# Optimization experiments

Measured on AMD Instinct MI355X. Metric: run time of the kernel, lower is better.

## Reference

```python
import jax, jax.numpy as jnp
import numpy as np

B, T, C = 4, 2048, 2048
N_HEAD = 16
HEAD_DIM = C // N_HEAD
ROPE_BASE = 10000.0


def setup_inputs() -> dict:
    key = jax.random.key(0)
    k1, k2, k3 = jax.random.split(key, 3)
    x = jax.random.normal(k1, (B, T, C), dtype=jnp.float32)
    Wqkv = jax.random.normal(k2, (C, 3 * C), dtype=jnp.float32) * 0.02
    bqkv = jnp.zeros((3 * C,), dtype=jnp.float32)
    Wproj = jax.random.normal(k3, (C, C), dtype=jnp.float32) * 0.02
    bproj = jnp.zeros((C,), dtype=jnp.float32)
    return {"x": x, "Wqkv": Wqkv, "bqkv": bqkv, "Wproj": Wproj, "bproj": bproj}


def _rope_cos_sin(seq_len, head_dim, dtype):
    inv_freq = 1.0 / (ROPE_BASE ** (jnp.arange(0, head_dim, 2, dtype=jnp.float32) / head_dim))
    t = jnp.arange(seq_len, dtype=jnp.float32)
    freqs = jnp.einsum("i,j->ij", t, inv_freq)          # [T, D/2]
    emb = jnp.concatenate([freqs, freqs], axis=-1)       # [T, D]
    return jnp.cos(emb).astype(dtype), jnp.sin(emb).astype(dtype)


def _rotate_half(x):
    half = x.shape[-1] // 2
    x1, x2 = x[..., :half], x[..., half:]
    return jnp.concatenate([-x2, x1], axis=-1)


def reference(x, Wqkv, bqkv, Wproj, bproj):
    b, t, c = x.shape
    qkv = x @ Wqkv + bqkv                                # [B, T, 3C]
    q, k, v = jnp.split(qkv, 3, axis=-1)
    # [B, T, C] -> [B, H, T, D]
    def to_heads(u):
        return u.reshape(b, t, N_HEAD, HEAD_DIM).transpose(0, 2, 1, 3)
    q, k, v = to_heads(q), to_heads(k), to_heads(v)
    cos, sin = _rope_cos_sin(t, HEAD_DIM, x.dtype)       # [T, D]
    cos = cos[None, None]                                # [1, 1, T, D]
    sin = sin[None, None]
    q = q * cos + _rotate_half(q) * sin
    k = k * cos + _rotate_half(k) * sin
    scale = 1.0 / np.sqrt(HEAD_DIM).astype(np.float32)
    scores = jnp.einsum("bhqd,bhkd->bhqk", q, k) * scale  # [B, H, T, T]
    causal = jnp.tril(jnp.ones((t, t), dtype=bool))
    scores = jnp.where(causal[None, None], scores, jnp.finfo(scores.dtype).min)
    att = jax.nn.softmax(scores, axis=-1)
    y = jnp.einsum("bhqk,bhkd->bhqd", att, v)             # [B, H, T, D]
    y = y.transpose(0, 2, 1, 3).reshape(b, t, c)
    return y @ Wproj + bproj
```

## Files before the change

### kernel.cpp

```cpp
#include <hip/hip_runtime.h>
#include <hip/hip_bf16.h>
#include <stdint.h>
#include <math.h>

#define NB 4
#define NT 2048
#define NC 2048
#define NH 16
#define HD 128
#define BT (NB*NT)

typedef __attribute__((ext_vector_type(8))) short s16x8;
typedef __attribute__((ext_vector_type(4))) short s16x4;
typedef __attribute__((ext_vector_type(4))) float f32x4;

typedef __attribute__((address_space(1))) void as1_void;
typedef __attribute__((address_space(3))) void as3_void;

static __device__ __forceinline__ unsigned short f2bf(float f) {
  union { float f; uint32_t u; } v; v.f = f;
  return (unsigned short)((v.u + 0x7fffu + ((v.u >> 16) & 1u)) >> 16);
}
static __device__ __forceinline__ float bf2f(unsigned short u) {
  union { uint32_t u; float f; } v; v.u = ((uint32_t)u) << 16;
  return v.f;
}
static __device__ __forceinline__ void async16(unsigned short* lds, const unsigned short* g) {
  __builtin_amdgcn_global_load_lds((as1_void*)g, (as3_void*)lds, 16, 0, 0);
}
static __device__ __forceinline__ uint32_t lds_off(void* p) {
  return (uint32_t)(size_t)(as3_void*)p;
}

__global__ void k_convert_bf16(const float* __restrict__ in, unsigned short* __restrict__ out, int n8) {
  int i = blockIdx.x * blockDim.x + threadIdx.x;
  if (i >= n8) return;
  const float4* p = (const float4*)in + (size_t)i * 2;
  float4 a = p[0], b = p[1];
  union { unsigned short s[8]; uint4 u; } o;
  o.s[0] = f2bf(a.x); o.s[1] = f2bf(a.y); o.s[2] = f2bf(a.z); o.s[3] = f2bf(a.w);
  o.s[4] = f2bf(b.x); o.s[5] = f2bf(b.y); o.s[6] = f2bf(b.z); o.s[7] = f2bf(b.w);
  ((uint4*)out)[i] = o.u;
}

__global__ void k_transpose_bf16(const float* __restrict__ W, unsigned short* __restrict__ WT, int K, int N) {
  __shared__ unsigned short tile[64][65];
  const int k0 = blockIdx.y * 64, n0 = blockIdx.x * 64;
  const int t = threadIdx.x;
  const int jj = t & 63, base_i = t >> 6;
  #pragma unroll
  for (int p = 0; p < 16; ++p) {
    int i = p * 4 + base_i;
    tile[i][jj] = f2bf(W[(size_t)(k0 + i) * N + n0 + jj]);
  }
  __syncthreads();
  #pragma unroll
  for (int p = 0; p < 16; ++p) {
    int j = p * 4 + base_i;
    WT[(size_t)(n0 + j) * K + k0 + jj] = tile[jj][j];
  }
}

__global__ void k_rope(unsigned short* __restrict__ Q, unsigned short* __restrict__ Kb) {
  int idx = blockIdx.x * 256 + threadIdx.x;
  int g = idx & 7;
  int tpos = (idx >> 3) & (NT - 1);
  int bh = idx >> 14;
  size_t o = ((size_t)bh * NT + tpos) * HD + g * 8;
  s16x8 qlo = *(const s16x8*)(Q + o),  qhi = *(const s16x8*)(Q + o + 64);
  s16x8 klo = *(const s16x8*)(Kb + o), khi = *(const s16x8*)(Kb + o + 64);
  s16x8 oql, oqh, okl, okh;
  const float qs = 0.08838834764831845f * 1.4426950408889634f;
  #pragma unroll
  for (int e = 0; e < 8; ++e) {
    const int d = g * 8 + e;
    float invf = exp2f(-(float)d * 0.2076205059304602f);
    float ang = (float)tpos * invf;
    float s, c;
    __sincosf(ang, &s, &c);
    float q1 = bf2f((unsigned short)qlo[e]), q2 = bf2f((unsigned short)qhi[e]);
    float k1 = bf2f((unsigned short)klo[e]), k2 = bf2f((unsigned short)khi[e]);
    oql[e] = (short)f2bf((q1 * c - q2 * s) * qs);
    oqh[e] = (short)f2bf((q2 * c + q1 * s) * qs);
    okl[e] = (short)f2bf(k1 * c - k2 * s);
    okh[e] = (short)f2bf(k2 * c + k1 * s);
  }
  *(s16x8*)(Q + o)       = oql;
  *(s16x8*)(Q + o + 64)  = oqh;
  *(s16x8*)(Kb + o)      = okl;
  *(s16x8*)(Kb + o + 64) = okh;
}

template<int MODE>
__global__ __launch_bounds__(256, 2)
void k_gemm_bt2(const unsigned short* __restrict__ A,
                const unsigned short* __restrict__ Bt,
                const float* __restrict__ bias,
                float* __restrict__ OutF,
                unsigned short* __restrict__ Qd,
                unsigned short* __restrict__ Kd,
                unsigned short* __restrict__ Vd,
                int M, int N, int K)
{
  __shared__ __align__(16) unsigned short Al[256 * 64];
  __shared__ __align__(16) unsigned short Bl[128 * 64];
  const int t = threadIdx.x;
  const int l = t & 63;
  const int wv = t >> 6;
  const int wm = wv >> 1, wn = wv & 1;
  const int gx = gridDim.x;
  const int lin = blockIdx.y * gx + blockIdx.x;
  const int qch = (gx * gridDim.y) >> 3;
  const int nid = (lin & 7) * qch + (lin >> 3);
  const int bm = (nid / gx) * 256, bn = (nid % gx) * 128;
  const int lr = l & 15, lg = l >> 4;

  f32x4 acc[8][4];
  #pragma unroll
  for (int i = 0; i < 8; ++i)
    #pragma unroll
    for (int j = 0; j < 4; ++j)
      acc[i][j] = f32x4{0.f, 0.f, 0.f, 0.f};

  for (int k0 = 0; k0 < K; k0 += 64) {
    #pragma unroll
    for (int i = 0; i < 8; ++i) {
      const int Cc = i * 256 + t;
      const int row = Cc >> 3;
      const int kc = (Cc & 7) ^ (row & 7);
      async16(&Al[(i * 256 + (t & 192)) * 8], &A[(size_t)(bm + row) * K + k0 + kc * 8]);
    }
    #pragma unroll
    for (int i = 0; i < 4; ++i) {
      const int Cc = i * 256 + t;
      const int row = Cc >> 3;
      const int kc = (Cc & 7) ^ (row & 7);
      async16(&Bl[(i * 256 + (t & 192)) * 8], &Bt[(size_t)(bn + row) * K + k0 + kc * 8]);
    }
    __syncthreads();
    #pragma unroll
    for (int kk = 0; kk < 2; ++kk) {
      s16x8 af[8], bfr[4];
      #pragma unroll
      for (int mi = 0; mi < 8; ++mi) {
        const int row = wm * 128 + mi * 16 + lr;
        const int ch = (kk * 4 + lg) ^ (row & 7);
        af[mi] = *(const s16x8*)&Al[row * 64 + ch * 8];
      }
      #pragma unroll
      for (int ni = 0; ni < 4; ++ni) {
        const int row = wn * 64 + ni * 16 + lr;
        const int ch = (kk * 4 + lg) ^ (row & 7);
        bfr[ni] = *(const s16x8*)&Bl[row * 64 + ch * 8];
      }
      __builtin_amdgcn_s_setprio(1);
      #pragma unroll
      for (int mi = 0; mi < 8; ++mi)
        #pragma unroll
        for (int ni = 0; ni < 4; ++ni)
          acc[mi][ni] = __builtin_amdgcn_mfma_f32_16x16x32_bf16(af[mi], bfr[ni], acc[mi][ni], 0, 0, 0);
      __builtin_amdgcn_s_setprio(0);
    }
    __syncthreads();
  }

  #pragma unroll
  for (int mi = 0; mi < 8; ++mi) {
    #pragma unroll
    for (int ni = 0; ni < 4; ++ni) {
      const int col = bn + wn * 64 + ni * 16 + lr;
      const float bv = bias[col];
      #pragma unroll
      for (int r = 0; r < 4; ++r) {
        const int row = bm + wm * 128 + mi * 16 + lg * 4 + r;
        const float v = acc[mi][ni][r] + bv;
        if (MODE == 1) {
          OutF[(size_t)row * N + col] = v;
        } else {
          const int which = col >> 11;
          const int cc = col & 2047;
          const int h = cc >> 7, d = cc & 127;
          const int b = row >> 11, tp = row & 2047;
          unsigned short* dst = (which == 0) ? Qd : (which == 1 ? Kd : Vd);
          dst[(((size_t)(b * NH + h)) * NT + tp) * HD + d] = f2bf(v);
        }
      }
    }
  }
}

__global__ __launch_bounds__(256, 2)
void k_attn(const unsigned short* __restrict__ Q,
            const unsigned short* __restrict__ Kg,
            const unsigned short* __restrict__ Vg,
            unsigned short* __restrict__ Yatt)
{
  __shared__ __align__(16) unsigned short Kl[2][64 * 128];
  __shared__ __align__(16) unsigned short Vl[2][64 * 128];
  const int bh = blockIdx.x;
  const int pair = blockIdx.y;
  const int b = bh >> 4, h = bh & 15;
  const int t = threadIdx.x, l = t & 63, wv = t >> 6;
  const int lr = l & 15, lg = l >> 4;
  const size_t hoff = (size_t)bh * NT * HD;
  const unsigned short* Qh = Q + hoff;
  const unsigned short* Kh = Kg + hoff;
  const unsigned short* Vh = Vg + hoff;
  const uint32_t vbase0 = lds_off(&Vl[0][0]);

  auto stageKV = [&](int buf, int kv0) {
    #pragma unroll
    for (int i = 0; i < 4; ++i) {
      const int Cc = i * 256 + t;
      {
        const int krow = Cc >> 4;
        const int kc = (Cc & 15) ^ (krow & 7);
        async16(&Kl[buf][(i * 256 + (t & 192)) * 8], &Kh[(size_t)(kv0 + krow) * HD + kc * 8]);
      }
      {
        const int S = Cc >> 3, c8 = Cc & 7;
        const int kq = S >> 3, dq = S & 7;
        const int vk = kq * 4 + (c8 >> 1), vd = dq * 16 + (c8 & 1) * 8;
        async16(&Vl[buf][(i * 256 + (t & 192)) * 8], &Vh[(size_t)(kv0 + vk) * HD + vd]);
      }
    }
  };

  #pragma unroll 1
  for (int rep = 0; rep < 2; ++rep) {
    const int qb16 = rep ? (15 - pair) : pair;
    const int q0w = qb16 * 128 + wv * 32;
    const int qrowA = q0w + lr, qrowB = q0w + 16 + lr;

    __syncthreads();

    s16x8 qfA[4], qfB[4];
    #pragma unroll
    for (int m = 0; m < 4; ++m) {
      qfA[m] = *(const s16x8*)(Qh + (size_t)qrowA * HD + m * 32 + lg * 8);
      qfB[m] = *(const s16x8*)(Qh + (size_t)qrowB * HD + m * 32 + lg * 8);
    }

    f32x4 ytA[8], ytB[8];
    #pragma unroll
    for (int n = 0; n < 8; ++n) { ytA[n] = f32x4{0.f,0.f,0.f,0.f}; ytB[n] = f32x4{0.f,0.f,0.f,0.f}; }
    float mrunA = -1e30f, lrunA = 0.f, mrunB = -1e30f, lrunB = 0.f;

    auto computeTile = [&](int buf, int kv0) {
      f32x4 stA[4], stB[4];
      __builtin_amdgcn_s_setprio(1);
      #pragma unroll
      for (int kt = 0; kt < 4; ++kt) {
        f32x4 a = f32x4{0.f,0.f,0.f,0.f}, bq = f32x4{0.f,0.f,0.f,0.f};
        const int krow = kt * 16 + lr;
        #pragma unroll
        for (int m = 0; m < 4; ++m) {
          const int ch = (m * 4 + lg) ^ (krow & 7);
          s16x8 kf = *(const s16x8*)&Kl[buf][krow * 128 + ch * 8];
          a  = __builtin_amdgcn_mfma_f32_16x16x32_bf16(kf, qfA[m], a, 0, 0, 0);
          bq = __builtin_amdgcn_mfma_f32_16x16x32_bf16(kf, qfB[m], bq, 0, 0, 0);
        }
        stA[kt] = a; stB[kt] = bq;
      }
      __builtin_amdgcn_s_setprio(0);

      if (kv0 + 63 > q0w) {
        #pragma unroll
        for (int kt = 0; kt < 4; ++kt)
          #pragma unroll
          for (int r = 0; r < 4; ++r) {
            const int key = kv0 + kt * 16 + lg * 4 + r;
            if (key > qrowA) stA[kt][r] = -3.0e38f;
            if (key > qrowB) stB[kt][r] = -3.0e38f;
          }
      }

      float tmA = -3.0e38f, tmB = -3.0e38f;
      #pragma unroll
      for (int kt = 0; kt < 4; ++kt)
        #pragma unroll
        for (int r = 0; r < 4; ++r) { tmA = fmaxf(tmA, stA[kt][r]); tmB = fmaxf(tmB, stB[kt][r]); }
      tmA = fmaxf(tmA, __shfl_xor(tmA, 16)); tmA = fmaxf(tmA, __shfl_xor(tmA, 32));
      tmB = fmaxf(tmB, __shfl_xor(tmB, 16)); tmB = fmaxf(tmB, __shfl_xor(tmB, 32));
      if (!__all((tmA - mrunA <= 8.0f) && (tmB - mrunB <= 8.0f))) {
        const float mnA = fmaxf(mrunA, tmA), mnB = fmaxf(mrunB, tmB);
        const float fsA = exp2f(mrunA - mnA), fsB = exp2f(mrunB - mnB);
        mrunA = mnA; mrunB = mnB;
        lrunA *= fsA; lrunB *= fsB;
        #pragma unroll
        for (int n = 0; n < 8; ++n)
          #pragma unroll
          for (int r = 0; r < 4; ++r) { ytA[n][r] *= fsA; ytB[n][r] *= fsB; }
      }

      float pvA[16], pvB[16];
      float psA = 0.f, psB = 0.f;
      #pragma unroll
      for (int kt = 0; kt < 4; ++kt)
        #pragma unroll
        for (int r = 0; r < 4; ++r) {
          const float pa = exp2f(stA[kt][r] - mrunA);
          const float pb = exp2f(stB[kt][r] - mrunB);
          psA += pa; psB += pb;
          pvA[kt * 4 + r] = pa; pvB[kt * 4 + r] = pb;
        }
      lrunA += psA; lrunB += psB;

      union { uint32_t w[4]; s16x8 v; } puA[2], puB[2];
      #pragma unroll
      for (int gk = 0; gk < 2; ++gk)
        #pragma unroll
        for (int w = 0; w < 4; ++w) {
          const int i0 = (gk * 2 + (w >> 1)) * 4 + (w & 1) * 2;
          asm("v_cvt_pk_bf16_f32 %0, %1, %2" : "=v"(puA[gk].w[w]) : "v"(pvA[i0]), "v"(pvA[i0 + 1]));
          asm("v_cvt_pk_bf16_f32 %0, %1, %2" : "=v"(puB[gk].w[w]) : "v"(pvB[i0]), "v"(pvB[i0 + 1]));
        }

      const uint32_t vb = vbase0 + (uint32_t)buf * 16384;
      #pragma unroll
      for (int gk = 0; gk < 2; ++gk) {
        s16x4 va[8], vb2[8];
        #pragma unroll
        for (int n = 0; n < 8; ++n) {
          const uint32_t a0 = vb + ((uint32_t)((gk * 8 + lg) * 8 + n)) * 128 + (uint32_t)lr * 8;
          asm volatile("ds_read_b64_tr_b16 %0, %1" : "=v"(va[n])  : "v"(a0));
          asm volatile("ds_read_b64_tr_b16 %0, %1" : "=v"(vb2[n]) : "v"(a0 + 4096));
        }
        asm volatile("s_waitcnt lgkmcnt(0)" ::: "memory");
        __builtin_amdgcn_sched_barrier(0);
        __builtin_amdgcn_s_setprio(1);
        #pragma unroll
        for (int n = 0; n < 8; ++n) {
          s16x8 vf;
          vf[0] = va[n][0];  vf[1] = va[n][1];  vf[2] = va[n][2];  vf[3] = va[n][3];
          vf[4] = vb2[n][0]; vf[5] = vb2[n][1]; vf[6] = vb2[n][2]; vf[7] = vb2[n][3];
          ytA[n] = __builtin_amdgcn_mfma_f32_16x16x32_bf16(vf, puA[gk].v, ytA[n], 0, 0, 0);
          ytB[n] = __builtin_amdgcn_mfma_f32_16x16x32_bf16(vf, puB[gk].v, ytB[n], 0, 0, 0);
        }
        __builtin_amdgcn_s_setprio(0);
      }
    };

    const int nkv = 2 * qb16 + 2;
    stageKV(0, 0);
    asm volatile("s_waitcnt vmcnt(0)" ::: "memory");
    __syncthreads();
    int buf = 0;
    #pragma unroll 1
    for (int kv = 0; kv < nkv - 1; ++kv) {
      stageKV(buf ^ 1, (kv + 1) * 64);
      computeTile(buf, kv * 64);
      asm volatile("s_waitcnt vmcnt(0)" ::: "memory");
      __builtin_amdgcn_s_barrier();
      buf ^= 1;
    }
    computeTile(buf, (nkv - 1) * 64);

    lrunA += __shfl_xor(lrunA, 16); lrunA += __shfl_xor(lrunA, 32);
    lrunB += __shfl_xor(lrunB, 16); lrunB += __shfl_xor(lrunB, 32);
    const float invA = 1.f / lrunA, invB = 1.f / lrunB;
    unsigned short* yrowA = Yatt + (size_t)(b * NT + qrowA) * NC + h * HD;
    unsigned short* yrowB = Yatt + (size_t)(b * NT + qrowB) * NC + h * HD;
    #pragma unroll
    for (int n = 0; n < 8; ++n) {
      uint32_t u0, u1;
      asm("v_cvt_pk_bf16_f32 %0, %1, %2" : "=v"(u0) : "v"(ytA[n][0] * invA), "v"(ytA[n][1] * invA));
      asm("v_cvt_pk_bf16_f32 %0, %1, %2" : "=v"(u1) : "v"(ytA[n][2] * invA), "v"(ytA[n][3] * invA));
      uint2 pk; pk.x = u0; pk.y = u1;
      *(uint2*)(yrowA + n * 16 + lg * 4) = pk;
      asm("v_cvt_pk_bf16_f32 %0, %1, %2" : "=v"(u0) : "v"(ytB[n][0] * invB), "v"(ytB[n][1] * invB));
      asm("v_cvt_pk_bf16_f32 %0, %1, %2" : "=v"(u1) : "v"(ytB[n][2] * invB), "v"(ytB[n][3] * invB));
      pk.x = u0; pk.y = u1;
      *(uint2*)(yrowB + n * 16 + lg * 4) = pk;
    }
  }
}

extern "C" void kernel_launch(void* const* d_in, const int* in_sizes, int n_in,
                              void* d_out, int out_size, void* d_ws, size_t ws_size,
                              hipStream_t stream) {
  (void)in_sizes; (void)n_in; (void)out_size; (void)ws_size;
  const float* x     = (const float*)d_in[0];
  const float* Wqkv  = (const float*)d_in[1];
  const float* bqkv  = (const float*)d_in[2];
  const float* Wproj = (const float*)d_in[3];
  const float* bproj = (const float*)d_in[4];
  float* out = (float*)d_out;
  char* ws = (char*)d_ws;

  unsigned short* xb     = (unsigned short*)(ws);
  unsigned short* WqkvT  = (unsigned short*)(ws + 33554432);
  unsigned short* WprojT = (unsigned short*)(ws + 58720256);
  unsigned short* Qb     = (unsigned short*)(ws + 67108864);
  unsigned short* Kb     = (unsigned short*)(ws + 100663296);
  unsigned short* Vb     = (unsigned short*)(ws + 134217728);
  unsigned short* att    = xb;

  k_convert_bf16<<<dim3(8192), dim3(256), 0, stream>>>(x, xb, BT * NC / 8);
  k_transpose_bf16<<<dim3(96, 32), dim3(256), 0, stream>>>(Wqkv, WqkvT, NC, 3 * NC);
  k_transpose_bf16<<<dim3(32, 32), dim3(256), 0, stream>>>(Wproj, WprojT, NC, NC);
  k_gemm_bt2<0><<<dim3(48, 32), dim3(256), 0, stream>>>(xb, WqkvT, bqkv, nullptr, Qb, Kb, Vb, BT, 3 * NC, NC);
  k_rope<<<dim3(4096), dim3(256), 0, stream>>>(Qb, Kb);
  k_attn<<<dim3(64, 8), dim3(256), 0, stream>>>(Qb, Kb, Vb, att);
  k_gemm_bt2<1><<<dim3(16, 32), dim3(256), 0, stream>>>(att, WprojT, bproj, out, nullptr, nullptr, nullptr, BT, NC, NC);
}
```

Measured before the change: 413.8 us.

## Pipeline GEMM with triple-buffered async LDS ring and skip empty attention tile

Measured after the change: 453.9 us. 1.1x slower.

```diff
diff --git a/kernel.cpp b/kernel.cpp
--- a/kernel.cpp
+++ b/kernel.cpp
@@ -16,6 +16,8 @@
 
 typedef __attribute__((address_space(1))) void as1_void;
 typedef __attribute__((address_space(3))) void as3_void;
+
+#define CFENCE asm volatile("" ::: "memory")
 
 static __device__ __forceinline__ unsigned short f2bf(float f) {
   union { float f; uint32_t u; } v; v.f = f;
@@ -93,26 +95,22 @@
 
 template<int MODE>
 __global__ __launch_bounds__(256, 2)
-void k_gemm_bt2(const unsigned short* __restrict__ A,
-                const unsigned short* __restrict__ Bt,
-                const float* __restrict__ bias,
-                float* __restrict__ OutF,
-                unsigned short* __restrict__ Qd,
-                unsigned short* __restrict__ Kd,
-                unsigned short* __restrict__ Vd,
-                int M, int N, int K)
+void k_gemm_ring(const unsigned short* __restrict__ A,
+                 const unsigned short* __restrict__ Bt,
+                 const float* __restrict__ bias,
+                 float* __restrict__ OutF,
+                 unsigned short* __restrict__ Qd,
+                 unsigned short* __restrict__ Kd,
+                 unsigned short* __restrict__ Vd,
+                 int M, int N, int K)
 {
-  __shared__ __align__(16) unsigned short Al[256 * 64];
-  __shared__ __align__(16) unsigned short Bl[128 * 64];
+  __shared__ __align__(16) unsigned short As[3][8192];
+  __shared__ __align__(16) unsigned short Bs[3][4096];
   const int t = threadIdx.x;
   const int l = t & 63;
   const int wv = t >> 6;
   const int wm = wv >> 1, wn = wv & 1;
-  const int gx = gridDim.x;
-  const int lin = blockIdx.y * gx + blockIdx.x;
-  const int qch = (gx * gridDim.y) >> 3;
-  const int nid = (lin & 7) * qch + (lin >> 3);
-  const int bm = (nid / gx) * 256, bn = (nid % gx) * 128;
+  const int bm = blockIdx.y * 256, bn = blockIdx.x * 128;
   const int lr = l & 15, lg = l >> 4;
 
   f32x4 acc[8][4];
@@ -122,46 +120,64 @@
     for (int j = 0; j < 4; ++j)
       acc[i][j] = f32x4{0.f, 0.f, 0.f, 0.f};
 
-  for (int k0 = 0; k0 < K; k0 += 64) {
-    #pragma unroll
-    for (int i = 0; i < 8; ++i) {
-      const int Cc = i * 256 + t;
-      const int row = Cc >> 3;
-      const int kc = (Cc & 7) ^ (row & 7);
-      async16(&Al[(i * 256 + (t & 192)) * 8], &A[(size_t)(bm + row) * K + k0 + kc * 8]);
-    }
-    #pragma unroll
-    for (int i = 0; i < 4; ++i) {
-      const int Cc = i * 256 + t;
-      const int row = Cc >> 3;
-      const int kc = (Cc & 7) ^ (row & 7);
-      async16(&Bl[(i * 256 + (t & 192)) * 8], &Bt[(size_t)(bn + row) * K + k0 + kc * 8]);
-    }
-    __syncthreads();
-    #pragma unroll
-    for (int kk = 0; kk < 2; ++kk) {
-      s16x8 af[8], bfr[4];
-      #pragma unroll
-      for (int mi = 0; mi < 8; ++mi) {
-        const int row = wm * 128 + mi * 16 + lr;
-        const int ch = (kk * 4 + lg) ^ (row & 7);
-        af[mi] = *(const s16x8*)&Al[row * 64 + ch * 8];
-      }
-      #pragma unroll
-      for (int ni = 0; ni < 4; ++ni) {
-        const int row = wn * 64 + ni * 16 + lr;
-        const int ch = (kk * 4 + lg) ^ (row & 7);
-        bfr[ni] = *(const s16x8*)&Bl[row * 64 + ch * 8];
-      }
-      __builtin_amdgcn_s_setprio(1);
-      #pragma unroll
-      for (int mi = 0; mi < 8; ++mi)
-        #pragma unroll
-        for (int ni = 0; ni < 4; ++ni)
-          acc[mi][ni] = __builtin_amdgcn_mfma_f32_16x16x32_bf16(af[mi], bfr[ni], acc[mi][ni], 0, 0, 0);
-      __builtin_amdgcn_s_setprio(0);
-    }
-    __syncthreads();
+  int arow[4], akc[4];
+  #pragma unroll
+  for (int j = 0; j < 4; ++j) {
+    const int Cc = j * 256 + t;
+    const int lq = Cc >> 3;
+    const int vl = (Cc & 7) ^ (lq & 7);
+    arow[j] = 2 * lq + (vl >> 2);
+    akc[j] = vl & 3;
+  }
+
+  auto stage = [&](int s, int k0) {
+    #pragma unroll
+    for (int j = 0; j < 4; ++j)
+      async16(&As[s][(j * 256 + (t & 192)) * 8], &A[(size_t)(bm + arow[j]) * K + k0 + akc[j] * 8]);
+    #pragma unroll
+    for (int j = 0; j < 2; ++j)
+      async16(&Bs[s][(j * 256 + (t & 192)) * 8], &Bt[(size_t)(bn + arow[j]) * K + k0 + akc[j] * 8]);
+  };
+  auto compute = [&](int s) {
+    s16x8 af[8], bfr[4];
+    #pragma unroll
+    for (int mi = 0; mi < 8; ++mi) {
+      const int row = wm * 128 + mi * 16 + lr;
+      const int lq = row >> 1;
+      const int sl = (((row & 1) << 2) | lg) ^ (lq & 7);
+      af[mi] = *(const s16x8*)&As[s][lq * 64 + sl * 8];
+    }
+    #pragma unroll
+    for (int ni = 0; ni < 4; ++ni) {
+      const int row = wn * 64 + ni * 16 + lr;
+      const int lq = row >> 1;
+      const int sl = (((row & 1) << 2) | lg) ^ (lq & 7);
+      bfr[ni] = *(const s16x8*)&Bs[s][lq * 64 + sl * 8];
+    }
+    __builtin_amdgcn_s_setprio(1);
+    #pragma unroll
+    for (int mi = 0; mi < 8; ++mi)
+      #pragma unroll
+      for (int ni = 0; ni < 4; ++ni)
+        acc[mi][ni] = __builtin_amdgcn_mfma_f32_16x16x32_bf16(af[mi], bfr[ni], acc[mi][ni], 0, 0, 0);
+    __builtin_amdgcn_s_setprio(0);
+  };
+
+  stage(0, 0); stage(1, 32);
+  asm volatile("s_waitcnt vmcnt(6)" ::: "memory");
+  CFENCE; __builtin_amdgcn_s_barrier(); CFENCE;
+
+  const int nU = K >> 5;
+  int sr = 0;
+  #pragma unroll 1
+  for (int u = 0; u < nU; ++u) {
+    int s2 = sr + 2; if (s2 >= 3) s2 -= 3;
+    const int kn = (u + 2 < nU) ? ((u + 2) << 5) : 0;
+    stage(s2, kn);
+    compute(sr);
+    asm volatile("s_waitcnt vmcnt(6)" ::: "memory");
+    CFENCE; __builtin_amdgcn_s_barrier(); CFENCE;
+    sr = (sr + 1 == 3) ? 0 : sr + 1;
   }
 
   #pragma unroll
@@ -354,7 +370,8 @@
       __builtin_amdgcn_s_barrier();
       buf ^= 1;
     }
-    computeTile(buf, (nkv - 1) * 64);
+    if ((nkv - 1) * 64 <= q0w + 31)
+      computeTile(buf, (nkv - 1) * 64);
 
     lrunA += __shfl_xor(lrunA, 16); lrunA += __shfl_xor(lrunA, 32);
     lrunB += __shfl_xor(lrunB, 16); lrunB += __shfl_xor(lrunB, 32);
@@ -399,8 +416,8 @@
   k_convert_bf16<<<dim3(8192), dim3(256), 0, stream>>>(x, xb, BT * NC / 8);
   k_transpose_bf16<<<dim3(96, 32), dim3(256), 0, stream>>>(Wqkv, WqkvT, NC, 3 * NC);
   k_transpose_bf16<<<dim3(32, 32), dim3(256), 0, stream>>>(Wproj, WprojT, NC, NC);
-  k_gemm_bt2<0><<<dim3(48, 32), dim3(256), 0, stream>>>(xb, WqkvT, bqkv, nullptr, Qb, Kb, Vb, BT, 3 * NC, NC);
+  k_gemm_ring<0><<<dim3(48, 32), dim3(256), 0, stream>>>(xb, WqkvT, bqkv, nullptr, Qb, Kb, Vb, BT, 3 * NC, NC);
   k_rope<<<dim3(4096), dim3(256), 0, stream>>>(Qb, Kb);
   k_attn<<<dim3(64, 8), dim3(256), 0, stream>>>(Qb, Kb, Vb, att);
-  k_gemm_bt2<1><<<dim3(16, 32), dim3(256), 0, stream>>>(att, WprojT, bproj, out, nullptr, nullptr, nullptr, BT, NC, NC);
-}
+  k_gemm_ring<1><<<dim3(16, 32), dim3(256), 0, stream>>>(att, WprojT, bproj, out, nullptr, nullptr, nullptr, BT, NC, NC);
+}
```
